# Kernel optimization log

Hardware: AMD Instinct MI355X
Metric: run time of the kernel (lower is better)

The kernel has to match this reference:

```python
import jax, jax.numpy as jnp
import numpy as np

TEMPERATURE = 34.0
LEAKY_SLOPE = 0.2


def setup_inputs() -> dict:
    key = jax.random.key(0)
    ks = jax.random.split(key, 6)
    B, C, H, W = 16, 64, 256, 256
    K, O, I, kk = 4, 64, 64, 3
    hidden = int(C * 0.25) + 1  # attention2d hidden_planes = 17
    return {
        "x": jax.random.normal(ks[0], (B, C, H, W), dtype=jnp.float32),
        "fc1_w": jax.random.normal(ks[1], (hidden, C), dtype=jnp.float32) * 0.1,
        "fc2_w": jax.random.normal(ks[2], (K, hidden), dtype=jnp.float32) * 0.1,
        "fc2_b": jnp.zeros((K,), dtype=jnp.float32),
        "weight": jax.random.normal(ks[3], (K, O, I, kk, kk), dtype=jnp.float32) * 0.05,
        "bias_k": jax.random.normal(ks[4], (K, O), dtype=jnp.float32) * 0.01,
    }


def reference(x, fc1_w, fc2_w, fc2_b, weight, bias_k):
    # Dynamic_conv2d forward (stride=1, padding=1, dilation=1, groups=1)
    B, C, H, W = x.shape
    K, O, I, kh, kw = weight.shape

    # attention2d: global avg pool -> 1x1 conv -> LeakyReLU(0.2) -> 1x1 conv -> softmax(x/T)
    pooled = jnp.mean(x, axis=(2, 3))                      # [B, C]
    h = pooled @ fc1_w.T                                   # [B, hidden]
    h = jnp.where(h >= 0, h, LEAKY_SLOPE * h)
    logits = h @ fc2_w.T + fc2_b                           # [B, K]
    att = jax.nn.softmax(logits / TEMPERATURE, axis=1)     # [B, K]

    # per-sample aggregated kernels and biases
    agg_w = jnp.einsum('bk,koihw->boihw', att, weight).reshape(B * O, I, kh, kw)
    agg_b = att @ bias_k                                   # [B, O]

    # grouped-conv trick: [1, B*C, H, W] conv with feature_group_count=B
    x1 = x.reshape(1, B * C, H, W)
    out = jax.lax.conv_general_dilated(
        x1, agg_w,
        window_strides=(1, 1),
        padding=((1, 1), (1, 1)),
        feature_group_count=B,
        dimension_numbers=('NCHW', 'OIHW', 'NCHW'),
    )
    out = out.reshape(B, O, H, W) + agg_b[:, :, None, None]
    return out
```

## Files before the change

### kernel.cpp

```cpp
#include <hip/hip_runtime.h>
#include <cstddef>
#include <cstdint>

#define BATCH 16
#define CIN 64
#define COUT 64
#define HH 256
#define WW 256
#define HID 17
#define KNUM 4

#define TH 8
#define TW 32
#define XROWS (TH + 2)
#define XCOLS (TW + 2)
#define NPIX (XROWS * XCOLS)
#define XSTR 72
#define XSTR32 36

typedef __attribute__((ext_vector_type(4))) float f32x4;
typedef __attribute__((ext_vector_type(8))) short s16x8;

static __device__ __forceinline__ unsigned short f2bf(float f) {
    unsigned u = __builtin_bit_cast(unsigned, f);
    u += 0x7FFFu + ((u >> 16) & 1u);
    return (unsigned short)(u >> 16);
}

__global__ __launch_bounds__(256) void pool_kernel(const float* __restrict__ x,
                                                   float* __restrict__ pooled) {
    int bc = blockIdx.x;
    const float4* p = (const float4*)(x + (size_t)bc * (HH * WW));
    float s = 0.f;
    for (int idx = threadIdx.x; idx < HH * WW / 4; idx += 256) {
        float4 v = p[idx];
        s += v.x + v.y + v.z + v.w;
    }
    #pragma unroll
    for (int off = 32; off > 0; off >>= 1) s += __shfl_down(s, off, 64);
    __shared__ float wsum[4];
    int lane = threadIdx.x & 63, wvi = threadIdx.x >> 6;
    if (lane == 0) wsum[wvi] = s;
    __syncthreads();
    if (threadIdx.x == 0) {
        float t = wsum[0] + wsum[1] + wsum[2] + wsum[3];
        pooled[bc] = t * (1.0f / (HH * WW));
    }
}

__global__ __launch_bounds__(256) void att_kernel(const float* __restrict__ pooled,
                                                  const float* __restrict__ fc1_w,
                                                  const float* __restrict__ fc2_w,
                                                  const float* __restrict__ fc2_b,
                                                  const float* __restrict__ bias_k,
                                                  float* __restrict__ att,
                                                  float* __restrict__ agg_b) {
    __shared__ float h_lds[BATCH][HID];
    __shared__ float logit_lds[BATCH][KNUM];
    __shared__ float att_lds[BATCH][KNUM];
    for (int idx = threadIdx.x; idx < BATCH * HID; idx += 256) {
        int b = idx / HID, j = idx - b * HID;
        float s = 0.f;
        for (int c = 0; c < CIN; ++c) s += pooled[b * CIN + c] * fc1_w[j * CIN + c];
        h_lds[b][j] = (s >= 0.f) ? s : 0.2f * s;
    }
    __syncthreads();
    if (threadIdx.x < BATCH * KNUM) {
        int b = threadIdx.x / KNUM, k = threadIdx.x - b * KNUM;
        float s = fc2_b[k];
        for (int j = 0; j < HID; ++j) s += h_lds[b][j] * fc2_w[k * HID + j];
        logit_lds[b][k] = s * (1.0f / 34.0f);
    }
    __syncthreads();
    if (threadIdx.x < BATCH) {
        int b = threadIdx.x;
        float m = logit_lds[b][0];
        for (int k = 1; k < KNUM; ++k) m = fmaxf(m, logit_lds[b][k]);
        float e[KNUM];
        float sum = 0.f;
        for (int k = 0; k < KNUM; ++k) { e[k] = expf(logit_lds[b][k] - m); sum += e[k]; }
        float inv = 1.0f / sum;
        for (int k = 0; k < KNUM; ++k) {
            float a = e[k] * inv;
            att_lds[b][k] = a;
            att[b * KNUM + k] = a;
        }
    }
    __syncthreads();
    for (int idx = threadIdx.x; idx < BATCH * COUT; idx += 256) {
        int b = idx / COUT, o = idx - b * COUT;
        float s = 0.f;
        for (int k = 0; k < KNUM; ++k) s += att_lds[b][k] * bias_k[k * COUT + o];
        agg_b[idx] = s;
    }
}

__global__ __launch_bounds__(256) void aggw_kernel(const float* __restrict__ att,
                                                   const float* __restrict__ weight,
                                                   unsigned* __restrict__ agg_wb) {
    const int total = BATCH * 9 * COUT * (CIN / 2);
    const size_t kstride = (size_t)COUT * CIN * 9;
    for (int d = blockIdx.x * 256 + threadIdx.x; d < total; d += gridDim.x * 256) {
        int b = d / (9 * COUT * 32);
        int rem = d - b * (9 * COUT * 32);
        int t = rem / (COUT * 32);
        int rem2 = rem - t * (COUT * 32);
        int o = rem2 >> 5;
        int ip = rem2 & 31;
        int i = ip * 2;
        float a0 = att[b * KNUM + 0], a1 = att[b * KNUM + 1];
        float a2 = att[b * KNUM + 2], a3 = att[b * KNUM + 3];
        const float* w0 = weight + ((size_t)(o * CIN + i) * 9 + t);
        float s0 = a0 * w0[0] + a1 * w0[kstride] + a2 * w0[2 * kstride] + a3 * w0[3 * kstride];
        const float* w1 = w0 + 9;
        float s1 = a0 * w1[0] + a1 * w1[kstride] + a2 * w1[2 * kstride] + a3 * w1[3 * kstride];
        agg_wb[d] = (unsigned)f2bf(s0) | ((unsigned)f2bf(s1) << 16);
    }
}

__global__ __launch_bounds__(256) void conv_kernel(
    const float* __restrict__ x, const unsigned* __restrict__ agg_wb,
    const float* __restrict__ agg_b, float* __restrict__ out)
{
    __shared__ short xs[NPIX * XSTR];
    unsigned* xs32 = (unsigned*)xs;

    const int tid = threadIdx.x;
    const int lane = tid & 63;
    const int wv = tid >> 6;
    const int l15 = lane & 15;
    const int q = lane >> 4;
    const int b = blockIdx.z;
    const int r0 = blockIdx.y * TH;
    const int c0 = blockIdx.x * TW;

    {
        const float* xb = x + (size_t)b * CIN * HH * WW;
        #pragma unroll 4
        for (int ig = 0; ig < CIN / 4; ++ig) {
            const float* p0 = xb + (size_t)(4 * ig) * (HH * WW);
            for (int pix = tid; pix < NPIX; pix += 256) {
                int r = pix / XCOLS;
                int c = pix - r * XCOLS;
                int gr = r0 - 1 + r, gc = c0 - 1 + c;
                float v0 = 0.f, v1 = 0.f, v2 = 0.f, v3 = 0.f;
                if ((unsigned)gr < HH && (unsigned)gc < WW) {
                    int off = gr * WW + gc;
                    v0 = p0[off];
                    v1 = p0[off + HH * WW];
                    v2 = p0[off + 2 * HH * WW];
                    v3 = p0[off + 3 * HH * WW];
                }
                uint2 pk;
                pk.x = (unsigned)f2bf(v0) | ((unsigned)f2bf(v1) << 16);
                pk.y = (unsigned)f2bf(v2) | ((unsigned)f2bf(v3) << 16);
                *(uint2*)(xs32 + pix * XSTR32 + ig * 2) = pk;
            }
        }
    }
    __syncthreads();

    const unsigned* wb = agg_wb + (size_t)b * (9 * COUT * (CIN / 2));

    f32x4 acc[4][4];
    #pragma unroll
    for (int mt = 0; mt < 4; ++mt)
        #pragma unroll
        for (int nt = 0; nt < 4; ++nt)
            acc[mt][nt] = (f32x4){0.f, 0.f, 0.f, 0.f};

    for (int t = 0; t < 9; ++t) {
        const int dh = t / 3;
        const int dw = t - dh * 3;
        #pragma unroll
        for (int ic = 0; ic < 2; ++ic) {
            s16x8 af[4];
            #pragma unroll
            for (int mt = 0; mt < 4; ++mt)
                af[mt] = *(const s16x8*)(wb + ((t * COUT + mt * 16 + l15) * 32 + ic * 16 + q * 4));
            s16x8 bfr[4];
            #pragma unroll
            for (int nt = 0; nt < 4; ++nt) {
                int rr = nt >> 1, cc = nt & 1;
                int pix = (2 * wv + rr + dh) * XCOLS + cc * 16 + l15 + dw;
                bfr[nt] = *(const s16x8*)(xs + pix * XSTR + ic * 32 + q * 8);
            }
            #pragma unroll
            for (int mt = 0; mt < 4; ++mt)
                #pragma unroll
                for (int nt = 0; nt < 4; ++nt)
                    acc[mt][nt] = __builtin_amdgcn_mfma_f32_16x16x32_bf16(af[mt], bfr[nt], acc[mt][nt], 0, 0, 0);
        }
    }

    const float* bbp = agg_b + b * COUT;
    float* op = out + (size_t)b * COUT * HH * WW;
    #pragma unroll
    for (int mt = 0; mt < 4; ++mt) {
        #pragma unroll
        for (int rg = 0; rg < 4; ++rg) {
            int o = mt * 16 + q * 4 + rg;
            float bv = bbp[o];
            #pragma unroll
            for (int nt = 0; nt < 4; ++nt) {
                int rr = nt >> 1, cc = nt & 1;
                int row = r0 + 2 * wv + rr;
                int col = c0 + cc * 16 + l15;
                op[((size_t)o * HH + row) * WW + col] = acc[mt][nt][rg] + bv;
            }
        }
    }
}

extern "C" void kernel_launch(void* const* d_in, const int* in_sizes, int n_in,
                              void* d_out, int out_size, void* d_ws, size_t ws_size,
                              hipStream_t stream) {
    const float* x      = (const float*)d_in[0];
    const float* fc1_w  = (const float*)d_in[1];
    const float* fc2_w  = (const float*)d_in[2];
    const float* fc2_b  = (const float*)d_in[3];
    const float* weight = (const float*)d_in[4];
    const float* bias_k = (const float*)d_in[5];
    float* out = (float*)d_out;
    float* ws  = (float*)d_ws;

    float*    pooled = ws;
    float*    att    = ws + 1024;
    float*    agg_b  = ws + 1088;
    unsigned* agg_wb = (unsigned*)(ws + 2112);

    pool_kernel<<<dim3(BATCH * CIN), dim3(256), 0, stream>>>(x, pooled);
    att_kernel<<<dim3(1), dim3(256), 0, stream>>>(pooled, fc1_w, fc2_w, fc2_b, bias_k, att, agg_b);
    aggw_kernel<<<dim3(1152), dim3(256), 0, stream>>>(att, weight, agg_wb);
    conv_kernel<<<dim3(WW / TW, HH / TH, BATCH), dim3(256), 0, stream>>>(x, agg_wb, agg_b, out);
}
```

Before: 714.5 us.

## Pre-transpose input to padded NHWC bf16 fused with pooling, conv reads from global

Adds a transpose kernel that reads x once, converts it to a padded NHWC bf16 buffer in workspace, and accumulates the channel means with atomics. This fuses the pooling pass with the layout conversion. The attention and weight aggregation are merged into one kernel. A new conv kernel handles one output row per block, with a swizzled block order, and loads MFMA B fragments straight from the NHWC buffer instead of staging halos through LDS. It needs a large workspace (about 135MB) and keeps the old path as a fallback when the workspace is too small.

```diff
diff --git a/kernel.cpp b/kernel.cpp
--- a/kernel.cpp
+++ b/kernel.cpp
@@ -10,6 +10,191 @@
 #define HID 17
 #define KNUM 4
 
+typedef __attribute__((ext_vector_type(4))) float f32x4;
+typedef __attribute__((ext_vector_type(8))) short s16x8;
+
+static __device__ __forceinline__ unsigned short f2bf(float f) {
+    unsigned u = __builtin_bit_cast(unsigned, f);
+    u += 0x7FFFu + ((u >> 16) & 1u);
+    return (unsigned short)(u >> 16);
+}
+
+#define XROWSTR 16512
+#define XBSTR   4227072
+
+__global__ __launch_bounds__(256) void tpose_pool_kernel(const float* __restrict__ x,
+                                                         short* __restrict__ xpad,
+                                                         float* __restrict__ pooled) {
+    const int b = blockIdx.z;
+    const int r = blockIdx.y;
+    const int half = blockIdx.x;
+    const int tid = threadIdx.x;
+    const int wave = tid >> 6;
+    const int lane = tid & 63;
+    const int w4 = lane >> 3;
+    const int g  = lane & 7;
+    const int px0 = half * 128 + wave * 32 + w4 * 4;
+
+    const float* xb = x + (size_t)b * (CIN * HH * WW) + (size_t)r * WW + px0;
+    float4 v[8];
+    #pragma unroll
+    for (int gi = 0; gi < 8; ++gi)
+        v[gi] = *(const float4*)(xb + (size_t)(g * 8 + gi) * (HH * WW));
+
+    short* dst0 = xpad + ((size_t)b * 256 + r) * XROWSTR + (size_t)(1 + px0) * 64 + g * 8;
+    #pragma unroll
+    for (int j = 0; j < 4; ++j) {
+        float f[8];
+        f[0]=v[0][j]; f[1]=v[1][j]; f[2]=v[2][j]; f[3]=v[3][j];
+        f[4]=v[4][j]; f[5]=v[5][j]; f[6]=v[6][j]; f[7]=v[7][j];
+        uint4 pk;
+        pk.x = (unsigned)f2bf(f[0]) | ((unsigned)f2bf(f[1]) << 16);
+        pk.y = (unsigned)f2bf(f[2]) | ((unsigned)f2bf(f[3]) << 16);
+        pk.z = (unsigned)f2bf(f[4]) | ((unsigned)f2bf(f[5]) << 16);
+        pk.w = (unsigned)f2bf(f[6]) | ((unsigned)f2bf(f[7]) << 16);
+        *(uint4*)(dst0 + (size_t)j * 64) = pk;
+    }
+
+    float ps[8];
+    #pragma unroll
+    for (int gi = 0; gi < 8; ++gi) ps[gi] = v[gi].x + v[gi].y + v[gi].z + v[gi].w;
+    #pragma unroll
+    for (int off = 8; off < 64; off <<= 1)
+        #pragma unroll
+        for (int gi = 0; gi < 8; ++gi) ps[gi] += __shfl_xor(ps[gi], off, 64);
+
+    __shared__ float pl[4][64];
+    if (w4 == 0) {
+        #pragma unroll
+        for (int gi = 0; gi < 8; ++gi) pl[wave][g * 8 + gi] = ps[gi];
+    }
+    __syncthreads();
+    if (tid < 64)
+        atomicAdd(&pooled[b * 64 + tid], pl[0][tid] + pl[1][tid] + pl[2][tid] + pl[3][tid]);
+
+    if (tid < 8) {
+        short* pz = xpad + ((size_t)b * 256 + r) * XROWSTR + (size_t)(half ? 257 : 0) * 64 + tid * 8;
+        *(uint4*)pz = (uint4){0u, 0u, 0u, 0u};
+    }
+}
+
+__global__ __launch_bounds__(256) void att_aggw_kernel(const float* __restrict__ pooled,
+                                                       const float* __restrict__ fc1_w,
+                                                       const float* __restrict__ fc2_w,
+                                                       const float* __restrict__ fc2_b,
+                                                       const float* __restrict__ bias_k,
+                                                       const float* __restrict__ weight,
+                                                       float* __restrict__ agg_b,
+                                                       unsigned* __restrict__ agg_wb) {
+    const int t = blockIdx.x;
+    const int b = blockIdx.y;
+    const int tid = threadIdx.x;
+    __shared__ float h_l[HID];
+    __shared__ float att_l[KNUM];
+
+    if (tid < HID) {
+        float s = 0.f;
+        for (int c = 0; c < CIN; ++c) s += pooled[b * CIN + c] * fc1_w[tid * CIN + c];
+        s *= (1.0f / (HH * WW));
+        h_l[tid] = (s >= 0.f) ? s : 0.2f * s;
+    }
+    __syncthreads();
+    if (tid == 0) {
+        float lg[KNUM];
+        float m = -1e30f;
+        for (int k = 0; k < KNUM; ++k) {
+            float s = fc2_b[k];
+            for (int j = 0; j < HID; ++j) s += h_l[j] * fc2_w[k * HID + j];
+            lg[k] = s * (1.0f / 34.0f);
+            m = fmaxf(m, lg[k]);
+        }
+        float sum = 0.f;
+        for (int k = 0; k < KNUM; ++k) { lg[k] = expf(lg[k] - m); sum += lg[k]; }
+        float inv = 1.0f / sum;
+        for (int k = 0; k < KNUM; ++k) att_l[k] = lg[k] * inv;
+    }
+    __syncthreads();
+    const float a0 = att_l[0], a1 = att_l[1], a2 = att_l[2], a3 = att_l[3];
+
+    if (t == 0 && tid < COUT) {
+        float s = a0 * bias_k[tid] + a1 * bias_k[COUT + tid] +
+                  a2 * bias_k[2 * COUT + tid] + a3 * bias_k[3 * COUT + tid];
+        agg_b[b * COUT + tid] = s;
+    }
+
+    const size_t kstr = (size_t)COUT * CIN * 9;
+    unsigned* dst = agg_wb + (size_t)b * (9 * COUT * 32) + (size_t)t * (COUT * 32);
+    #pragma unroll
+    for (int e8 = 0; e8 < 8; ++e8) {
+        int e = tid * 8 + e8;
+        int o = e >> 5, ip = e & 31, i = 2 * ip;
+        const float* w0 = weight + ((size_t)(o * CIN + i) * 9 + t);
+        float s0 = a0 * w0[0] + a1 * w0[kstr] + a2 * w0[2 * kstr] + a3 * w0[3 * kstr];
+        const float* w1 = w0 + 9;
+        float s1 = a0 * w1[0] + a1 * w1[kstr] + a2 * w1[2 * kstr] + a3 * w1[3 * kstr];
+        dst[e] = (unsigned)f2bf(s0) | ((unsigned)f2bf(s1) << 16);
+    }
+}
+
+__global__ __launch_bounds__(256) void conv_nhwc_kernel(const short* __restrict__ xpad,
+                                                        const unsigned* __restrict__ agg_wb,
+                                                        const float* __restrict__ agg_b,
+                                                        float* __restrict__ out) {
+    const int swz = (blockIdx.x & 7) * 512 + (blockIdx.x >> 3);
+    const int b = swz >> 8;
+    const int r = swz & 255;
+    const int lane = threadIdx.x & 63;
+    const int wv = threadIdx.x >> 6;
+    const int l15 = lane & 15;
+    const int q = lane >> 4;
+    const int w0 = wv * 64;
+
+    const unsigned* wb = agg_wb + (size_t)b * (9 * COUT * 32);
+
+    f32x4 acc[4][4];
+    #pragma unroll
+    for (int mt = 0; mt < 4; ++mt)
+        #pragma unroll
+        for (int nt = 0; nt < 4; ++nt) acc[mt][nt] = (f32x4){0.f, 0.f, 0.f, 0.f};
+
+    for (int t = 0; t < 9; ++t) {
+        const int dh = t / 3;
+        const int dw = t - dh * 3;
+        const int rp = r + dh - 1;
+        if ((unsigned)rp >= HH) continue;
+        const short* xrow = xpad + ((size_t)b * 256 + rp) * XROWSTR;
+        #pragma unroll
+        for (int ic = 0; ic < 2; ++ic) {
+            s16x8 af[4];
+            #pragma unroll
+            for (int mt = 0; mt < 4; ++mt)
+                af[mt] = *(const s16x8*)(wb + ((size_t)(t * COUT + mt * 16 + l15) * 32 + ic * 16 + q * 4));
+            #pragma unroll
+            for (int nt = 0; nt < 4; ++nt) {
+                const short* bp = xrow + (size_t)(w0 + nt * 16 + l15 + dw) * 64 + ic * 32 + q * 8;
+                s16x8 bf = *(const s16x8*)bp;
+                #pragma unroll
+                for (int mt = 0; mt < 4; ++mt)
+                    acc[mt][nt] = __builtin_amdgcn_mfma_f32_16x16x32_bf16(af[mt], bf, acc[mt][nt], 0, 0, 0);
+            }
+        }
+    }
+
+    const float* bb = agg_b + b * COUT;
+    float* op = out + (size_t)b * (COUT * HH * WW) + (size_t)r * WW;
+    #pragma unroll
+    for (int mt = 0; mt < 4; ++mt) {
+        #pragma unroll
+        for (int rg = 0; rg < 4; ++rg) {
+            int o = mt * 16 + q * 4 + rg;
+            float bv = bb[o];
+            #pragma unroll
+            for (int nt = 0; nt < 4; ++nt)
+                op[(size_t)o * (HH * WW) + w0 + nt * 16 + l15] = acc[mt][nt][rg] + bv;
+        }
+    }
+}
+
 #define TH 8
 #define TW 32
 #define XROWS (TH + 2)
@@ -17,15 +202,6 @@
 #define NPIX (XROWS * XCOLS)
 #define XSTR 72
 #define XSTR32 36
-
-typedef __attribute__((ext_vector_type(4))) float f32x4;
-typedef __attribute__((ext_vector_type(8))) short s16x8;
-
-static __device__ __forceinline__ unsigned short f2bf(float f) {
-    unsigned u = __builtin_bit_cast(unsigned, f);
-    u += 0x7FFFu + ((u >> 16) & 1u);
-    return (unsigned short)(u >> 16);
-}
 
 __global__ __launch_bounds__(256) void pool_kernel(const float* __restrict__ x,
                                                    float* __restrict__ pooled) {
@@ -42,10 +218,8 @@
     int lane = threadIdx.x & 63, wvi = threadIdx.x >> 6;
     if (lane == 0) wsum[wvi] = s;
     __syncthreads();
-    if (threadIdx.x == 0) {
-        float t = wsum[0] + wsum[1] + wsum[2] + wsum[3];
-        pooled[bc] = t * (1.0f / (HH * WW));
-    }
+    if (threadIdx.x == 0)
+        pooled[bc] = (wsum[0] + wsum[1] + wsum[2] + wsum[3]) * (1.0f / (HH * WW));
 }
 
 __global__ __launch_bounds__(256) void att_kernel(const float* __restrict__ pooled,
@@ -76,15 +250,10 @@
         int b = threadIdx.x;
         float m = logit_lds[b][0];
         for (int k = 1; k < KNUM; ++k) m = fmaxf(m, logit_lds[b][k]);
-        float e[KNUM];
-        float sum = 0.f;
+        float e[KNUM], sum = 0.f;
         for (int k = 0; k < KNUM; ++k) { e[k] = expf(logit_lds[b][k] - m); sum += e[k]; }
         float inv = 1.0f / sum;
-        for (int k = 0; k < KNUM; ++k) {
-            float a = e[k] * inv;
-            att_lds[b][k] = a;
-            att[b * KNUM + k] = a;
-        }
+        for (int k = 0; k < KNUM; ++k) { att_lds[b][k] = e[k] * inv; att[b * KNUM + k] = e[k] * inv; }
     }
     __syncthreads();
     for (int idx = threadIdx.x; idx < BATCH * COUT; idx += 256) {
@@ -105,9 +274,7 @@
         int rem = d - b * (9 * COUT * 32);
         int t = rem / (COUT * 32);
         int rem2 = rem - t * (COUT * 32);
-        int o = rem2 >> 5;
-        int ip = rem2 & 31;
-        int i = ip * 2;
+        int o = rem2 >> 5, ip = rem2 & 31, i = ip * 2;
         float a0 = att[b * KNUM + 0], a1 = att[b * KNUM + 1];
         float a2 = att[b * KNUM + 2], a3 = att[b * KNUM + 3];
         const float* w0 = weight + ((size_t)(o * CIN + i) * 9 + t);
@@ -124,7 +291,6 @@
 {
     __shared__ short xs[NPIX * XSTR];
     unsigned* xs32 = (unsigned*)xs;
-
     const int tid = threadIdx.x;
     const int lane = tid & 63;
     const int wv = tid >> 6;
@@ -133,23 +299,19 @@
     const int b = blockIdx.z;
     const int r0 = blockIdx.y * TH;
     const int c0 = blockIdx.x * TW;
-
     {
         const float* xb = x + (size_t)b * CIN * HH * WW;
         #pragma unroll 4
         for (int ig = 0; ig < CIN / 4; ++ig) {
             const float* p0 = xb + (size_t)(4 * ig) * (HH * WW);
             for (int pix = tid; pix < NPIX; pix += 256) {
-                int r = pix / XCOLS;
-                int c = pix - r * XCOLS;
-                int gr = r0 - 1 + r, gc = c0 - 1 + c;
+                int rr = pix / XCOLS, cc = pix - rr * XCOLS;
+                int gr = r0 - 1 + rr, gc = c0 - 1 + cc;
                 float v0 = 0.f, v1 = 0.f, v2 = 0.f, v3 = 0.f;
                 if ((unsigned)gr < HH && (unsigned)gc < WW) {
                     int off = gr * WW + gc;
-                    v0 = p0[off];
-                    v1 = p0[off + HH * WW];
-                    v2 = p0[off + 2 * HH * WW];
-                    v3 = p0[off + 3 * HH * WW];
+                    v0 = p0[off]; v1 = p0[off + HH * WW];
+                    v2 = p0[off + 2 * HH * WW]; v3 = p0[off + 3 * HH * WW];
                 }
                 uint2 pk;
                 pk.x = (unsigned)f2bf(v0) | ((unsigned)f2bf(v1) << 16);
@@ -159,19 +321,14 @@
         }
     }
     __syncthreads();
-
     const unsigned* wb = agg_wb + (size_t)b * (9 * COUT * (CIN / 2));
-
     f32x4 acc[4][4];
     #pragma unroll
     for (int mt = 0; mt < 4; ++mt)
         #pragma unroll
-        for (int nt = 0; nt < 4; ++nt)
-            acc[mt][nt] = (f32x4){0.f, 0.f, 0.f, 0.f};
-
+        for (int nt = 0; nt < 4; ++nt) acc[mt][nt] = (f32x4){0.f, 0.f, 0.f, 0.f};
     for (int t = 0; t < 9; ++t) {
-        const int dh = t / 3;
-        const int dw = t - dh * 3;
+        const int dh = t / 3, dw = t - dh * 3;
         #pragma unroll
         for (int ic = 0; ic < 2; ++ic) {
             s16x8 af[4];
@@ -192,11 +349,10 @@
                     acc[mt][nt] = __builtin_amdgcn_mfma_f32_16x16x32_bf16(af[mt], bfr[nt], acc[mt][nt], 0, 0, 0);
         }
     }
-
     const float* bbp = agg_b + b * COUT;
     float* op = out + (size_t)b * COUT * HH * WW;
     #pragma unroll
-    for (int mt = 0; mt < 4; ++mt) {
+    for (int mt = 0; mt < 4; ++mt)
         #pragma unroll
         for (int rg = 0; rg < 4; ++rg) {
             int o = mt * 16 + q * 4 + rg;
@@ -204,12 +360,9 @@
             #pragma unroll
             for (int nt = 0; nt < 4; ++nt) {
                 int rr = nt >> 1, cc = nt & 1;
-                int row = r0 + 2 * wv + rr;
-                int col = c0 + cc * 16 + l15;
-                op[((size_t)o * HH + row) * WW + col] = acc[mt][nt][rg] + bv;
+                op[((size_t)o * HH + (r0 + 2 * wv + rr)) * WW + c0 + cc * 16 + l15] = acc[mt][nt][rg] + bv;
             }
         }
-    }
 }
 
 extern "C" void kernel_launch(void* const* d_in, const int* in_sizes, int n_in,
@@ -225,12 +378,25 @@
     float* ws  = (float*)d_ws;
 
     float*    pooled = ws;
-    float*    att    = ws + 1024;
-    float*    agg_b  = ws + 1088;
-    unsigned* agg_wb = (unsigned*)(ws + 2112);
-
-    pool_kernel<<<dim3(BATCH * CIN), dim3(256), 0, stream>>>(x, pooled);
-    att_kernel<<<dim3(1), dim3(256), 0, stream>>>(pooled, fc1_w, fc2_w, fc2_b, bias_k, att, agg_b);
-    aggw_kernel<<<dim3(1152), dim3(256), 0, stream>>>(att, weight, agg_wb);
-    conv_kernel<<<dim3(WW / TW, HH / TH, BATCH), dim3(256), 0, stream>>>(x, agg_wb, agg_b, out);
-}
+    float*    agg_b  = ws + 1024;
+    unsigned* agg_wb = (unsigned*)(ws + 2048);
+    short*    xpad   = (short*)(ws + 296960);
+    const size_t REQ = (size_t)296960 * 4 + (size_t)BATCH * 256 * 258 * 64 * 2;
+
+    if (ws_size >= REQ) {
+        hipMemsetAsync(pooled, 0, BATCH * CIN * sizeof(float), stream);
+        tpose_pool_kernel<<<dim3(2, 256, BATCH), dim3(256), 0, stream>>>(x, xpad, pooled);
+        att_aggw_kernel<<<dim3(9, BATCH), dim3(256), 0, stream>>>(pooled, fc1_w, fc2_w, fc2_b,
+                                                                  bias_k, weight, agg_b, agg_wb);
+        conv_nhwc_kernel<<<dim3(4096), dim3(256), 0, stream>>>(xpad, agg_wb, agg_b, out);
+    } else {
+        float* pooled2 = ws;
+        float* att2    = ws + 1024;
+        float* agg_b2  = ws + 1088;
+        unsigned* agg_wb2 = (unsigned*)(ws + 2112);
+        pool_kernel<<<dim3(BATCH * CIN), dim3(256), 0, stream>>>(x, pooled2);
+        att_kernel<<<dim3(1), dim3(256), 0, stream>>>(pooled2, fc1_w, fc2_w, fc2_b, bias_k, att2, agg_b2);
+        aggw_kernel<<<dim3(1152), dim3(256), 0, stream>>>(att2, weight, agg_wb2);
+        conv_kernel<<<dim3(WW / TW, HH / TH, BATCH), dim3(256), 0, stream>>>(x, agg_wb2, agg_b2, out);
+    }
+}
```

New measurement: 779.8 us. 1.09x slower.
